# Kernel optimization log

Hardware: AMD Instinct MI355X
Metric: run time of the kernel (lower is better)

Reference implementation:

```python
import jax, jax.numpy as jnp
import numpy as np

B, N, H, T = 128, 512, 128, 32


def setup_inputs() -> dict:
    key = jax.random.key(0)
    ks = jax.random.split(key, 6)
    s = 0.05  # small init scale keeps softmax logits sane
    return {
        "encoder_outputs": jax.random.normal(ks[0], (B, N, H), jnp.float32),
        "W_ih": jax.random.normal(ks[1], (4 * H, H), jnp.float32) * s,
        "W_hh": jax.random.normal(ks[2], (4 * H, H), jnp.float32) * s,
        "b_ih": jnp.zeros((4 * H,), jnp.float32),
        "b_hh": jnp.zeros((4 * H,), jnp.float32),
        "W1": jax.random.normal(ks[3], (H, H), jnp.float32) * s,
        "W2": jax.random.normal(ks[4], (H, H), jnp.float32) * s,
        "v": jax.random.normal(ks[5], (H,), jnp.float32) * s,
        "decode_steps": T,
    }


def reference(encoder_outputs, W_ih, W_hh, b_ih, b_hh, W1, W2, v, decode_steps):
    b, n, h = encoder_outputs.shape
    dtype = encoder_outputs.dtype
    # W1(encoder_outputs) is loop-invariant: hoist it (same math as the torch loop)
    enc_trans = jnp.einsum("bnh,kh->bnk", encoder_outputs, W1)  # [B,n,H]

    dec0 = encoder_outputs.mean(axis=1)  # [B,H]
    hx0 = jnp.zeros((b, h), dtype)
    cx0 = jnp.zeros((b, h), dtype)
    mask0 = jnp.zeros((b, n), bool)
    key0 = jax.random.key(42)
    rows = jnp.arange(b)

    def step(carry, _):
        dec_input, hx, cx, mask, key = carry
        # torch.nn.LSTMCell: gates ordered i, f, g, o
        gates = dec_input @ W_ih.T + b_ih + hx @ W_hh.T + b_hh  # [B,4H]
        i, f, g, o = jnp.split(gates, 4, axis=-1)
        i = jax.nn.sigmoid(i)
        f = jax.nn.sigmoid(f)
        g = jnp.tanh(g)
        o = jax.nn.sigmoid(o)
        cx_new = f * cx + i * g
        hx_new = o * jnp.tanh(cx_new)
        # additive attention scores
        dec_trans = hx_new @ W2.T  # [B,H]
        scores = jnp.einsum("bnh,h->bn", jnp.tanh(enc_trans + dec_trans[:, None, :]), v)
        scores = jnp.where(mask, -jnp.inf, scores)  # masked_fill(-inf)
        # sample next node (torch.multinomial on softmax == categorical on logits)
        key, sub = jax.random.split(key)
        idx = jax.random.categorical(sub, scores, axis=-1)  # [B]
        probs = jax.nn.softmax(scores, axis=-1)
        sel_log_prob = jnp.log(jnp.take_along_axis(probs, idx[:, None], axis=1)[:, 0] + 1e-9)
        mask_new = mask.at[rows, idx].set(True)
        dec_next = jnp.take_along_axis(encoder_outputs, idx[:, None, None], axis=1)[:, 0]  # [B,H]
        return (dec_next, hx_new, cx_new, mask_new, key), (idx, sel_log_prob)

    _, (tours, log_probs) = jax.lax.scan(
        step, (dec0, hx0, cx0, mask0, key0), xs=None, length=decode_steps
    )
    return tours.T, log_probs.T  # [B,T], [B,T]
```

## Files before the change

kernel.cpp:

```cpp
#include <hip/hip_runtime.h>
#include <cstdint>
#include <cstddef>


constexpr int B = 128, N = 512, H = 128, T = 32;
constexpr int G4 = 4 * H;
constexpr float TINYF = 1.17549435e-38f;

__host__ __device__ inline uint32_t rotl32(uint32_t v, int d) {
  return (v << d) | (v >> (32 - d));
}

__host__ __device__ inline void tf2x32(uint32_t k0, uint32_t k1,
                                       uint32_t x0, uint32_t x1,
                                       uint32_t& o0, uint32_t& o1) {
  uint32_t ks2 = k0 ^ k1 ^ 0x1BD11BDAu;
  x0 += k0; x1 += k1;
#define TF_R(r) x0 += x1; x1 = rotl32(x1, (r)); x1 ^= x0;
  TF_R(13) TF_R(15) TF_R(26) TF_R(6)
  x0 += k1; x1 += ks2 + 1u;
  TF_R(17) TF_R(29) TF_R(16) TF_R(24)
  x0 += ks2; x1 += k0 + 2u;
  TF_R(13) TF_R(15) TF_R(26) TF_R(6)
  x0 += k0; x1 += k1 + 3u;
  TF_R(17) TF_R(29) TF_R(16) TF_R(24)
  x0 += k1; x1 += ks2 + 4u;
  TF_R(13) TF_R(15) TF_R(26) TF_R(6)
  x0 += ks2; x1 += k0 + 5u;
#undef TF_R
  o0 = x0; o1 = x1;
}

struct KeyArgs { uint32_t k[2 * T]; };

static KeyArgs make_subkeys() {
  KeyArgs ka;
  uint32_t k0 = 0u, k1 = 42u;
  for (int t = 0; t < T; ++t) {
    uint32_t n0, n1, s0, s1;
    tf2x32(k0, k1, 0u, 0u, n0, n1);
    tf2x32(k0, k1, 0u, 1u, s0, s1);
    ka.k[2 * t] = s0; ka.k[2 * t + 1] = s1;
    k0 = n0; k1 = n1;
  }
  return ka;
}

__device__ inline uint32_t gumbel_bits(uint32_t sk0, uint32_t sk1, int i) {
  uint32_t o0, o1;
  tf2x32(sk0, sk1, 0u, (uint32_t)i, o0, o1);
  return o0 ^ o1;
}

__device__ inline float fast_tanh(float x) {
  float cx = fminf(9.0f, fmaxf(-9.0f, x));
  float t = __expf(2.0f * cx);
  return (t - 1.0f) * __builtin_amdgcn_rcpf(t + 1.0f);
}

__global__ void k_transpose(const float* __restrict__ Wih, const float* __restrict__ Whh,
                            const float* __restrict__ W2, const float* __restrict__ W1,
                            float* __restrict__ WihT, float* __restrict__ WhhT,
                            float* __restrict__ W2T, float* __restrict__ W1T) {
  int i = blockIdx.x * blockDim.x + threadIdx.x;
  if (i < H * G4) {
    int h = i >> 9, j = i & (G4 - 1);
    WihT[i] = Wih[j * H + h];
  } else if (i < 2 * H * G4) {
    int q = i - H * G4; int h = q >> 9, j = q & (G4 - 1);
    WhhT[q] = Whh[j * H + h];
  } else if (i < 2 * H * G4 + H * H) {
    int q = i - 2 * H * G4; int h = q >> 7, k = q & (H - 1);
    W2T[q] = W2[k * H + h];
  } else if (i < 2 * H * G4 + 2 * H * H) {
    int q = i - 2 * H * G4 - H * H; int h = q >> 7, k = q & (H - 1);
    W1T[q] = W1[k * H + h];
  }
}

__global__ __launch_bounds__(256) void k_enc_trans(const float* __restrict__ enc,
                                                   const float* __restrict__ W1T,
                                                   float* __restrict__ encT2) {
  __shared__ __align__(16) float es[16 * 128];
  int blk = blockIdx.x;
  int b = blk >> 5;
  int n0 = (blk & 31) << 4;
  const float* src = enc + ((size_t)b * N + n0) * H;
  for (int i = threadIdx.x; i < 16 * 128; i += 256) es[i] = src[i];
  __syncthreads();
  int k = threadIdx.x & 127, ng = threadIdx.x >> 7;
  float acc[8] = {0.f, 0.f, 0.f, 0.f, 0.f, 0.f, 0.f, 0.f};
  for (int h = 0; h < H; h += 4) {
    float w0 = W1T[(h + 0) * H + k];
    float w1 = W1T[(h + 1) * H + k];
    float w2 = W1T[(h + 2) * H + k];
    float w3 = W1T[(h + 3) * H + k];
#pragma unroll
    for (int j = 0; j < 8; ++j) {
      const float4 e = *(const float4*)&es[(ng * 8 + j) * 128 + h];
      acc[j] += w0 * e.x + w1 * e.y + w2 * e.z + w3 * e.w;
    }
  }
  float* dst = encT2 + (size_t)b * H * N + (size_t)k * N + n0 + ng * 8;
  ((float4*)dst)[0] = make_float4(acc[0], acc[1], acc[2], acc[3]);
  ((float4*)dst)[1] = make_float4(acc[4], acc[5], acc[6], acc[7]);
}

__global__ __launch_bounds__(1024) void k_decode(
    const float* __restrict__ enc, const float* __restrict__ encT2,
    const float* __restrict__ WihT, const float* __restrict__ WhhT,
    const float* __restrict__ W2T,
    const float* __restrict__ bih, const float* __restrict__ bhh,
    const float* __restrict__ v,
    KeyArgs keys, float* __restrict__ out) {
  __shared__ __align__(16) float xs[H];
  __shared__ __align__(16) float hs[H];
  __shared__ __align__(16) float cs[H];
  __shared__ __align__(16) float dt[H];
  __shared__ __align__(16) float vv[H];
  __shared__ __align__(16) float bsum[G4];
  __shared__ float pg[2][G4];
  __shared__ float ps[2][N];
  __shared__ float pdt[4][H];
  __shared__ float sc[N];
  __shared__ float wr_z[8], wr_m[8], wr_s[8];
  __shared__ int wr_i[8];
  __shared__ float s_smax;
  __shared__ int s_idx;

  const int tid = threadIdx.x;
  const int b = blockIdx.x;
  const int lane = tid & 63;
  const int wave = tid >> 6;
  const int half = tid >> 9;
  const int id = tid & 511;

  if (tid < 512) {
    int h = tid & 127, part = tid >> 7;
    float s = 0.f;
    const float* p = enc + ((size_t)b * N + part * 128) * H + h;
#pragma unroll 8
    for (int n = 0; n < 128; ++n) s += p[(size_t)n * H];
    pdt[part][h] = s;
    bsum[tid] = bih[tid] + bhh[tid];
  }
  if (tid < 128) { hs[tid] = 0.f; cs[tid] = 0.f; vv[tid] = v[tid]; }
  __syncthreads();
  if (tid < 128)
    xs[tid] = (pdt[0][tid] + pdt[1][tid] + pdt[2][tid] + pdt[3][tid]) * (1.0f / N);
  bool masked = false;
  __syncthreads();

  for (int t = 0; t < T; ++t) {
    {
      const float* wi = WihT + (size_t)(half * 64) * G4 + id;
      const float* wh = WhhT + (size_t)(half * 64) * G4 + id;
      const int hb = half * 64;
      float a0 = 0.f, a1 = 0.f;
#pragma unroll 8
      for (int h = 0; h < 64; ++h) {
        a0 += wi[h * G4] * xs[hb + h];
        a1 += wh[h * G4] * hs[hb + h];
      }
      pg[half][id] = a0 + a1;
    }
    __syncthreads();
    if (tid < 128) {
      float gi = pg[0][tid] + pg[1][tid] + bsum[tid];
      float gf = pg[0][H + tid] + pg[1][H + tid] + bsum[H + tid];
      float gg = pg[0][2 * H + tid] + pg[1][2 * H + tid] + bsum[2 * H + tid];
      float go = pg[0][3 * H + tid] + pg[1][3 * H + tid] + bsum[3 * H + tid];
      gi = 1.0f / (1.0f + expf(-gi));
      gf = 1.0f / (1.0f + expf(-gf));
      gg = tanhf(gg);
      go = 1.0f / (1.0f + expf(-go));
      float c = gf * cs[tid] + gi * gg;
      cs[tid] = c;
      hs[tid] = go * tanhf(c);
    }
    __syncthreads();
    if (tid < 512) {
      int k = tid & 127, part = tid >> 7;
      const float* w2 = W2T + (size_t)(part * 32) * H + k;
      const int hb = part * 32;
      float a = 0.f;
#pragma unroll 8
      for (int h = 0; h < 32; ++h) a += w2[h * H] * hs[hb + h];
      pdt[part][k] = a;
    }
    __syncthreads();
    if (tid < 128) dt[tid] = pdt[0][tid] + pdt[1][tid] + pdt[2][tid] + pdt[3][tid];
    __syncthreads();
    {
      const int kb = half * 64;
      const float* ep = encT2 + (size_t)b * (H * N) + (size_t)kb * N + id;
      float a0 = 0.f, a1 = 0.f;
#pragma unroll 8
      for (int kk = 0; kk < 64; kk += 2) {
        float e0 = ep[(size_t)kk * N];
        float e1 = ep[(size_t)(kk + 1) * N];
        a0 += vv[kb + kk] * fast_tanh(e0 + dt[kb + kk]);
        a1 += vv[kb + kk + 1] * fast_tanh(e1 + dt[kb + kk + 1]);
      }
      ps[half][id] = a0 + a1;
    }
    __syncthreads();
    if (tid < 512) {
      float s = masked ? -INFINITY : (ps[0][tid] + ps[1][tid]);
      sc[tid] = s;
      uint32_t bits = gumbel_bits(keys.k[2 * t], keys.k[2 * t + 1], b * N + tid);
      float f = __uint_as_float((bits >> 9) | 0x3f800000u) - 1.0f;
      float u = fmaxf(TINYF, f + TINYF);
      float g = -logf(-logf(u));
      float z = s + g;
      int zi = tid;
      float m = s;
#pragma unroll
      for (int d = 32; d >= 1; d >>= 1) {
        float oz = __shfl_xor(z, d);
        int oi = __shfl_xor(zi, d);
        float om = __shfl_xor(m, d);
        if (oz > z || (oz == z && oi < zi)) { z = oz; zi = oi; }
        m = fmaxf(m, om);
      }
      if (lane == 0) { wr_z[wave] = z; wr_i[wave] = zi; wr_m[wave] = m; }
    }
    __syncthreads();
    if (tid == 0) {
      float bz = wr_z[0]; int bi = wr_i[0]; float bm = wr_m[0];
#pragma unroll
      for (int w = 1; w < 8; ++w) {
        if (wr_z[w] > bz || (wr_z[w] == bz && wr_i[w] < bi)) { bz = wr_z[w]; bi = wr_i[w]; }
        bm = fmaxf(bm, wr_m[w]);
      }
      s_idx = bi; s_smax = bm;
    }
    __syncthreads();
    if (tid < 512) {
      float e = expf(sc[tid] - s_smax);
#pragma unroll
      for (int d = 32; d >= 1; d >>= 1) e += __shfl_xor(e, d);
      if (lane == 0) wr_s[wave] = e;
      if (tid == s_idx) masked = true;
    } else if (tid < 640) {
      xs[tid - 512] = enc[((size_t)b * N + s_idx) * H + (tid - 512)];
    }
    __syncthreads();
    if (tid == 0) {
      float sum = wr_s[0] + wr_s[1] + wr_s[2] + wr_s[3]
                + wr_s[4] + wr_s[5] + wr_s[6] + wr_s[7];
      float p = expf(sc[s_idx] - s_smax) / sum;
      out[(size_t)b * T + t] = (float)s_idx;
      out[(size_t)B * T + (size_t)b * T + t] = logf(p + 1e-9f);
    }
    __syncthreads();
  }
}

extern "C" void kernel_launch(void* const* d_in, const int* in_sizes, int n_in,
                              void* d_out, int out_size, void* d_ws, size_t ws_size,
                              hipStream_t stream) {
  (void)in_sizes; (void)n_in; (void)out_size; (void)ws_size;
  const float* enc = (const float*)d_in[0];
  const float* Wih = (const float*)d_in[1];
  const float* Whh = (const float*)d_in[2];
  const float* bih = (const float*)d_in[3];
  const float* bhh = (const float*)d_in[4];
  const float* W1  = (const float*)d_in[5];
  const float* W2  = (const float*)d_in[6];
  const float* v   = (const float*)d_in[7];
  float* out = (float*)d_out;
  float* ws = (float*)d_ws;

  float* WihT  = ws;
  float* WhhT  = ws + 65536;
  float* W2T   = ws + 131072;
  float* W1T   = ws + 147456;
  float* encT2 = ws + 163840;

  KeyArgs keys = make_subkeys();

  k_transpose<<<640, 256, 0, stream>>>(Wih, Whh, W2, W1, WihT, WhhT, W2T, W1T);
  k_enc_trans<<<B * N / 16, 256, 0, stream>>>(enc, W1T, encT2);
  k_decode<<<B, 1024, 0, stream>>>(enc, encT2, WihT, WhhT, W2T, bih, bhh, v, keys, out);
}
```

Before: 615.5 us.

## Split each batch row's decode across two workgroups with global-memory flag exchange

The decode kernel now runs two 512-thread workgroups per batch row, each scoring half of the 512 nodes. Per step they exchange partial argmax, max and sum-exp through agent-scope atomics in workspace and spin on a flag, so the logsumexp is combined across the two halves. The aim is to use 256 workgroups instead of 128 on the many CUs and to shorten the attention-score phase. Each workgroup still redundantly computes the LSTM and W2 projections. The spin-wait needs both workgroups of a pair to be resident at the same time, and the flag slots reuse the W1T workspace area, which is dead once enc_trans has run.

```diff
diff --git a/kernel.cpp b/kernel.cpp
--- a/kernel.cpp
+++ b/kernel.cpp
@@ -6,6 +6,7 @@
 constexpr int B = 128, N = 512, H = 128, T = 32;
 constexpr int G4 = 4 * H;
 constexpr float TINYF = 1.17549435e-38f;
+constexpr uint32_t FLAG_BASE = 0x5AFE0000u;
 
 __host__ __device__ inline uint32_t rotl32(uint32_t v, int d) {
   return (v << d) | (v >> (32 - d));
@@ -56,6 +57,13 @@
   float cx = fminf(9.0f, fmaxf(-9.0f, x));
   float t = __expf(2.0f * cx);
   return (t - 1.0f) * __builtin_amdgcn_rcpf(t + 1.0f);
+}
+
+__device__ inline void ag_store(uint32_t* p, uint32_t v) {
+  __hip_atomic_store(p, v, __ATOMIC_RELAXED, __HIP_MEMORY_SCOPE_AGENT);
+}
+__device__ inline uint32_t ag_load(const uint32_t* p) {
+  return __hip_atomic_load(p, __ATOMIC_RELAXED, __HIP_MEMORY_SCOPE_AGENT);
 }
 
 __global__ void k_transpose(const float* __restrict__ Wih, const float* __restrict__ Whh,
@@ -106,39 +114,37 @@
   ((float4*)dst)[1] = make_float4(acc[4], acc[5], acc[6], acc[7]);
 }
 
-__global__ __launch_bounds__(1024) void k_decode(
+__global__ __launch_bounds__(512) void k_decode(
     const float* __restrict__ enc, const float* __restrict__ encT2,
     const float* __restrict__ WihT, const float* __restrict__ WhhT,
     const float* __restrict__ W2T,
     const float* __restrict__ bih, const float* __restrict__ bhh,
     const float* __restrict__ v,
-    KeyArgs keys, float* __restrict__ out) {
+    KeyArgs keys, uint32_t* __restrict__ slots, float* __restrict__ out) {
   __shared__ __align__(16) float xs[H];
   __shared__ __align__(16) float hs[H];
   __shared__ __align__(16) float cs[H];
   __shared__ __align__(16) float dt[H];
   __shared__ __align__(16) float vv[H];
   __shared__ __align__(16) float bsum[G4];
-  __shared__ float pg[2][G4];
-  __shared__ float ps[2][N];
+  __shared__ float gates[G4];
   __shared__ float pdt[4][H];
-  __shared__ float sc[N];
-  __shared__ float wr_z[8], wr_m[8], wr_s[8];
-  __shared__ int wr_i[8];
-  __shared__ float s_smax;
+  __shared__ float ps[2][256];
+  __shared__ float sc[256];
+  __shared__ float wr_z[4], wr_m[4], wr_s[4];
+  __shared__ int wr_i[4];
   __shared__ int s_idx;
 
   const int tid = threadIdx.x;
-  const int b = blockIdx.x;
+  const int bq = blockIdx.x >> 1;
+  const int nh = blockIdx.x & 1;
   const int lane = tid & 63;
   const int wave = tid >> 6;
-  const int half = tid >> 9;
-  const int id = tid & 511;
-
-  if (tid < 512) {
+
+  {
     int h = tid & 127, part = tid >> 7;
     float s = 0.f;
-    const float* p = enc + ((size_t)b * N + part * 128) * H + h;
+    const float* p = enc + ((size_t)bq * N + part * 128) * H + h;
 #pragma unroll 8
     for (int n = 0; n < 128; ++n) s += p[(size_t)n * H];
     pdt[part][h] = s;
@@ -151,25 +157,29 @@
   bool masked = false;
   __syncthreads();
 
+  uint32_t* my = slots + (((bq << 1) | nh) << 3);
+  uint32_t* th = slots + (((bq << 1) | (nh ^ 1)) << 3);
+
   for (int t = 0; t < T; ++t) {
     {
-      const float* wi = WihT + (size_t)(half * 64) * G4 + id;
-      const float* wh = WhhT + (size_t)(half * 64) * G4 + id;
-      const int hb = half * 64;
-      float a0 = 0.f, a1 = 0.f;
+      const float* wi = WihT + tid;
+      const float* wh = WhhT + tid;
+      float ax0 = 0.f, ah0 = 0.f, ax1 = 0.f, ah1 = 0.f;
 #pragma unroll 8
       for (int h = 0; h < 64; ++h) {
-        a0 += wi[h * G4] * xs[hb + h];
-        a1 += wh[h * G4] * hs[hb + h];
-      }
-      pg[half][id] = a0 + a1;
+        ax0 += wi[h * G4] * xs[h];
+        ah0 += wh[h * G4] * hs[h];
+        ax1 += wi[(64 + h) * G4] * xs[64 + h];
+        ah1 += wh[(64 + h) * G4] * hs[64 + h];
+      }
+      gates[tid] = (ax0 + ah0) + (ax1 + ah1);
     }
     __syncthreads();
     if (tid < 128) {
-      float gi = pg[0][tid] + pg[1][tid] + bsum[tid];
-      float gf = pg[0][H + tid] + pg[1][H + tid] + bsum[H + tid];
-      float gg = pg[0][2 * H + tid] + pg[1][2 * H + tid] + bsum[2 * H + tid];
-      float go = pg[0][3 * H + tid] + pg[1][3 * H + tid] + bsum[3 * H + tid];
+      float gi = gates[tid] + bsum[tid];
+      float gf = gates[H + tid] + bsum[H + tid];
+      float gg = gates[2 * H + tid] + bsum[2 * H + tid];
+      float go = gates[3 * H + tid] + bsum[3 * H + tid];
       gi = 1.0f / (1.0f + expf(-gi));
       gf = 1.0f / (1.0f + expf(-gf));
       gg = tanhf(gg);
@@ -179,7 +189,7 @@
       hs[tid] = go * tanhf(c);
     }
     __syncthreads();
-    if (tid < 512) {
+    {
       int k = tid & 127, part = tid >> 7;
       const float* w2 = W2T + (size_t)(part * 32) * H + k;
       const int hb = part * 32;
@@ -192,8 +202,9 @@
     if (tid < 128) dt[tid] = pdt[0][tid] + pdt[1][tid] + pdt[2][tid] + pdt[3][tid];
     __syncthreads();
     {
-      const int kb = half * 64;
-      const float* ep = encT2 + (size_t)b * (H * N) + (size_t)kb * N + id;
+      const int kh = tid >> 8, ni = tid & 255;
+      const int kb = kh * 64;
+      const float* ep = encT2 + (size_t)bq * (H * N) + (size_t)kb * N + nh * 256 + ni;
       float a0 = 0.f, a1 = 0.f;
 #pragma unroll 8
       for (int kk = 0; kk < 64; kk += 2) {
@@ -202,18 +213,19 @@
         a0 += vv[kb + kk] * fast_tanh(e0 + dt[kb + kk]);
         a1 += vv[kb + kk + 1] * fast_tanh(e1 + dt[kb + kk + 1]);
       }
-      ps[half][id] = a0 + a1;
-    }
-    __syncthreads();
-    if (tid < 512) {
+      ps[kh][ni] = a0 + a1;
+    }
+    __syncthreads();
+    if (tid < 256) {
+      const int ng = nh * 256 + tid;
       float s = masked ? -INFINITY : (ps[0][tid] + ps[1][tid]);
       sc[tid] = s;
-      uint32_t bits = gumbel_bits(keys.k[2 * t], keys.k[2 * t + 1], b * N + tid);
+      uint32_t bits = gumbel_bits(keys.k[2 * t], keys.k[2 * t + 1], bq * N + ng);
       float f = __uint_as_float((bits >> 9) | 0x3f800000u) - 1.0f;
       float u = fmaxf(TINYF, f + TINYF);
       float g = -logf(-logf(u));
       float z = s + g;
-      int zi = tid;
+      int zi = ng;
       float m = s;
 #pragma unroll
       for (int d = 32; d >= 1; d >>= 1) {
@@ -223,35 +235,54 @@
         if (oz > z || (oz == z && oi < zi)) { z = oz; zi = oi; }
         m = fmaxf(m, om);
       }
-      if (lane == 0) { wr_z[wave] = z; wr_i[wave] = zi; wr_m[wave] = m; }
+      float e = expf(s - m);
+#pragma unroll
+      for (int d = 32; d >= 1; d >>= 1) e += __shfl_xor(e, d);
+      if (lane == 0) { wr_z[wave] = z; wr_i[wave] = zi; wr_m[wave] = m; wr_s[wave] = e; }
     }
     __syncthreads();
     if (tid == 0) {
       float bz = wr_z[0]; int bi = wr_i[0]; float bm = wr_m[0];
 #pragma unroll
-      for (int w = 1; w < 8; ++w) {
+      for (int w = 1; w < 4; ++w) {
         if (wr_z[w] > bz || (wr_z[w] == bz && wr_i[w] < bi)) { bz = wr_z[w]; bi = wr_i[w]; }
         bm = fmaxf(bm, wr_m[w]);
       }
-      s_idx = bi; s_smax = bm;
-    }
-    __syncthreads();
-    if (tid < 512) {
-      float e = expf(sc[tid] - s_smax);
-#pragma unroll
-      for (int d = 32; d >= 1; d >>= 1) e += __shfl_xor(e, d);
-      if (lane == 0) wr_s[wave] = e;
-      if (tid == s_idx) masked = true;
-    } else if (tid < 640) {
-      xs[tid - 512] = enc[((size_t)b * N + s_idx) * H + (tid - 512)];
-    }
-    __syncthreads();
-    if (tid == 0) {
-      float sum = wr_s[0] + wr_s[1] + wr_s[2] + wr_s[3]
-                + wr_s[4] + wr_s[5] + wr_s[6] + wr_s[7];
-      float p = expf(sc[s_idx] - s_smax) / sum;
-      out[(size_t)b * T + t] = (float)s_idx;
-      out[(size_t)B * T + (size_t)b * T + t] = logf(p + 1e-9f);
+      float es = wr_s[0] * expf(wr_m[0] - bm) + wr_s[1] * expf(wr_m[1] - bm)
+               + wr_s[2] * expf(wr_m[2] - bm) + wr_s[3] * expf(wr_m[3] - bm);
+      float scat = sc[bi - nh * 256];
+      ag_store(my + 0, __float_as_uint(bz));
+      ag_store(my + 1, (uint32_t)bi);
+      ag_store(my + 2, __float_as_uint(bm));
+      ag_store(my + 3, __float_as_uint(es));
+      ag_store(my + 4, __float_as_uint(scat));
+      __hip_atomic_store(my + 7, FLAG_BASE + (uint32_t)t,
+                         __ATOMIC_RELEASE, __HIP_MEMORY_SCOPE_AGENT);
+      while (__hip_atomic_load(th + 7, __ATOMIC_ACQUIRE, __HIP_MEMORY_SCOPE_AGENT)
+             != FLAG_BASE + (uint32_t)t)
+        __builtin_amdgcn_s_sleep(1);
+      float oz = __uint_as_float(ag_load(th + 0));
+      int oi = (int)ag_load(th + 1);
+      float om = __uint_as_float(ag_load(th + 2));
+      float oes = __uint_as_float(ag_load(th + 3));
+      float oscat = __uint_as_float(ag_load(th + 4));
+      bool iwin = (bz > oz) || (bz == oz && bi < oi);
+      int idx = iwin ? bi : oi;
+      s_idx = idx;
+      if (nh == 0) {
+        float M = fmaxf(bm, om);
+        float sum = es * expf(bm - M) + oes * expf(om - M);
+        float scidx = iwin ? scat : oscat;
+        float p = expf(scidx - M) / sum;
+        out[(size_t)bq * T + t] = (float)idx;
+        out[(size_t)B * T + (size_t)bq * T + t] = logf(p + 1e-9f);
+      }
+    }
+    __syncthreads();
+    if (tid < 256) {
+      if (tid == s_idx - nh * 256) masked = true;
+    } else if (tid < 384) {
+      xs[tid - 256] = enc[((size_t)bq * N + s_idx) * H + (tid - 256)];
     }
     __syncthreads();
   }
@@ -277,10 +308,12 @@
   float* W2T   = ws + 131072;
   float* W1T   = ws + 147456;
   float* encT2 = ws + 163840;
+  uint32_t* slots = (uint32_t*)W1T;
 
   KeyArgs keys = make_subkeys();
 
   k_transpose<<<640, 256, 0, stream>>>(Wih, Whh, W2, W1, WihT, WhhT, W2T, W1T);
   k_enc_trans<<<B * N / 16, 256, 0, stream>>>(enc, W1T, encT2);
-  k_decode<<<B, 1024, 0, stream>>>(enc, encT2, WihT, WhhT, W2T, bih, bhh, v, keys, out);
-}
+  k_decode<<<2 * B, 512, 0, stream>>>(enc, encT2, WihT, WhhT, W2T, bih, bhh, v,
+                                      keys, slots, out);
+}
```

Result: slower. 711.0 us (+15.5%).
